# Performance work log

Hardware: AMD Instinct MI355X
Metric: run time of the kernel (lower is better)

## Reference

```python
import jax, jax.numpy as jnp
import numpy as np
from functools import partial

D_MODEL = 1024
D_STATE = 16
D_CONV = 4
EXPAND = 2
DIM = EXPAND * D_MODEL  # 2048


def setup_inputs() -> dict:
    key = jax.random.key(0)
    ks = jax.random.split(key, 10)
    s = lambda fan_in: 1.0 / np.sqrt(fan_in)
    inp = {
        "x": jax.random.normal(ks[0], (8, 2048, D_MODEL), dtype=jnp.float32),
        "W_in": jax.random.normal(ks[1], (DIM, D_MODEL), dtype=jnp.float32) * s(D_MODEL),
        "b_in": jnp.zeros((DIM,), dtype=jnp.float32),
        "conv_w": jax.random.normal(ks[2], (DIM, 1, D_CONV), dtype=jnp.float32) * s(D_CONV),
        "conv_b": jnp.zeros((DIM,), dtype=jnp.float32),
        "W_x": jax.random.normal(ks[3], (3 * D_STATE, DIM), dtype=jnp.float32) * s(DIM),
        "W_dt": jax.random.normal(ks[4], (DIM, D_STATE), dtype=jnp.float32) * s(D_STATE),
        "b_dt": jnp.zeros((DIM,), dtype=jnp.float32),
        "W_out": jax.random.normal(ks[5], (D_MODEL, DIM), dtype=jnp.float32) * s(DIM),
        "b_out": jnp.zeros((D_MODEL,), dtype=jnp.float32),
    }
    return inp


def _selective_scan(xc, delta, A, Bm, Cm):
    # xc, delta: (B, L, DIM); Bm, Cm: (B, L, N); A: (N,)
    Bsz = xc.shape[0]
    h0 = jnp.zeros((Bsz, DIM, D_STATE), dtype=xc.dtype)

    def step(h, inputs):
        xc_t, d_t, b_t, c_t = inputs  # (B,DIM),(B,DIM),(B,N),(B,N)
        h = h * jnp.exp(d_t[:, :, None] * A) + xc_t[:, :, None] * b_t[:, None, :]
        y_t = jnp.einsum("bdn,bn->bd", h, c_t)
        return h, y_t

    tm = lambda a: jnp.swapaxes(a, 0, 1)  # time-major
    _, ys = jax.lax.scan(step, h0, (tm(xc), tm(delta), tm(Bm), tm(Cm)))
    return jnp.swapaxes(ys, 0, 1)  # (B, L, DIM)


def reference(x, W_in, b_in, conv_w, conv_b, W_x, W_dt, b_dt, W_out, b_out):
    A = -jnp.exp(jnp.linspace(0.0, -5.0, D_STATE).astype(x.dtype))  # (N,)
    xp = x @ W_in.T + b_in  # (B, L, DIM)
    # depthwise conv1d, padding=D_CONV-1 on BOTH sides (as torch Conv1d) -> length L+D_CONV-1
    xc = jax.lax.conv_general_dilated(
        jnp.swapaxes(xp, 1, 2), conv_w,
        window_strides=(1,), padding=[(D_CONV - 1, D_CONV - 1)],
        feature_group_count=DIM,
        dimension_numbers=("NCH", "OIH", "NCH"),
    ) + conv_b[None, :, None]
    xc = jnp.swapaxes(xc, 1, 2)  # (B, Lc, DIM)
    x_dbl = xc @ W_x.T  # (B, Lc, 3N)
    d_raw, Bm, Cm = jnp.split(x_dbl, [D_STATE, 2 * D_STATE], axis=-1)
    delta = jax.nn.softplus(d_raw @ W_dt.T + b_dt)  # (B, Lc, DIM)
    y = _selective_scan(xc, delta, A, Bm, Cm)  # (B, Lc, DIM)
    return y @ W_out.T + b_out  # (B, Lc, D_MODEL)
```

## Files before the change

### kernel.cpp

```cpp
#include <hip/hip_runtime.h>
#include <cstdint>
#include <cstddef>

#define B8 8
#define LSEQ 2048
#define LC 2051
#define DMODEL 1024
#define DIM 2048
#define LPAD 2054
#define M2 16408
#define M2P 16512
#define CS 32
#define NCH 65

typedef __attribute__((ext_vector_type(8))) short short8;
typedef __attribute__((ext_vector_type(4))) float floatx4;
typedef __attribute__((ext_vector_type(2))) float float2v;

__device__ __constant__ float AeT[16] = {
  -1.0f,          -0.71653131f, -0.51341712f, -0.36787944f,
  -0.26359714f,   -0.18887560f, -0.13533528f, -0.09697208f,
  -0.06948345f,   -0.04978707f, -0.03567399f, -0.02556154f,
  -0.01831564f,   -0.01312373f, -0.00940356f, -0.00673795f};

#define LOG2E 1.44269504088896f

__device__ __forceinline__ float bf2f(unsigned short h) {
  union { unsigned int u; float f; } v; v.u = ((unsigned int)h) << 16; return v.f;
}
__device__ __forceinline__ unsigned short f2bf(float f) {
  union { float f; unsigned int u; } v; v.f = f;
  unsigned int r = (v.u + 0x7FFFu + ((v.u >> 16) & 1u)) >> 16;
  return (unsigned short)r;
}

__device__ __forceinline__ float2v pk_mul_vv(float2v a, float2v b) {
  float2v d; asm("v_pk_mul_f32 %0, %1, %2" : "=v"(d) : "v"(a), "v"(b)); return d;
}
__device__ __forceinline__ float2v pk_mul_sv(float2v bs, float2v a) {
  float2v d; asm("v_pk_mul_f32 %0, %1, %2" : "=v"(d) : "s"(bs), "v"(a)); return d;
}
__device__ __forceinline__ float2v pk_fma_vvv(float2v a, float2v b, float2v c) {
  float2v d; asm("v_pk_fma_f32 %0, %1, %2, %3" : "=v"(d) : "v"(a), "v"(b), "v"(c)); return d;
}
__device__ __forceinline__ float2v pk_fma_vsv(float2v a, float2v bs, float2v c) {
  float2v d; asm("v_pk_fma_f32 %0, %1, %2, %3" : "=v"(d) : "v"(a), "s"(bs), "v"(c)); return d;
}
__device__ __forceinline__ float2v pk_add_vv(float2v a, float2v b) {
  float2v d; asm("v_pk_add_f32 %0, %1, %2" : "=v"(d) : "v"(a), "v"(b)); return d;
}
__device__ __forceinline__ float exp2_raw(float x) {
  float d; asm("v_exp_f32 %0, %1" : "=v"(d) : "v"(x)); return d;
}

__global__ __launch_bounds__(256) void cvt_f32_bf16(const float* __restrict__ in,
                                                    unsigned short* __restrict__ out,
                                                    int n8) {
  int i = blockIdx.x * 256 + threadIdx.x;
  if (i >= n8) return;
  const float4* p = (const float4*)in + (size_t)i * 2;
  float4 a = p[0], b = p[1];
  uint4 o;
  o.x = (unsigned)f2bf(a.x) | ((unsigned)f2bf(a.y) << 16);
  o.y = (unsigned)f2bf(a.z) | ((unsigned)f2bf(a.w) << 16);
  o.z = (unsigned)f2bf(b.x) | ((unsigned)f2bf(b.y) << 16);
  o.w = (unsigned)f2bf(b.z) | ((unsigned)f2bf(b.w) << 16);
  *((uint4*)out + i) = o;
}

__global__ __launch_bounds__(256) void zero_pads(unsigned short* __restrict__ xp) {
  int i = blockIdx.x * 256 + threadIdx.x;
  int b = i / 1536;
  int r6 = (i % 1536) / 256;
  int dd = (i % 256) * 8;
  int row = (r6 < 3) ? r6 : (2048 + r6);
  uint4 z = make_uint4(0, 0, 0, 0);
  *(uint4*)(xp + ((size_t)b * LPAD + row) * DIM + dd) = z;
}

__global__ __launch_bounds__(256) void conv_kernel(const unsigned short* __restrict__ xp,
                                                   const float* __restrict__ conv_w,
                                                   const float* __restrict__ conv_b,
                                                   unsigned short* __restrict__ xc) {
  const int tc = blockIdx.x, b = blockIdx.y;
  const int d0 = threadIdx.x * 8;
  const unsigned short* base = xp + ((size_t)b * LPAD + tc) * DIM + d0;

  float4 cw[8];
#pragma unroll
  for (int j = 0; j < 8; ++j) cw[j] = *(const float4*)(conv_w + (size_t)(d0 + j) * 4);

  float acc[8];
  const float4* cb4 = (const float4*)(conv_b + d0);
  float4 cb0 = cb4[0], cb1 = cb4[1];
  acc[0] = cb0.x; acc[1] = cb0.y; acc[2] = cb0.z; acc[3] = cb0.w;
  acc[4] = cb1.x; acc[5] = cb1.y; acc[6] = cb1.z; acc[7] = cb1.w;

#pragma unroll
  for (int k = 0; k < 4; ++k) {
    uint4 v = *(const uint4*)(base + (size_t)k * DIM);
    unsigned short e[8];
    e[0] = v.x & 0xffff; e[1] = v.x >> 16; e[2] = v.y & 0xffff; e[3] = v.y >> 16;
    e[4] = v.z & 0xffff; e[5] = v.z >> 16; e[6] = v.w & 0xffff; e[7] = v.w >> 16;
#pragma unroll
    for (int j = 0; j < 8; ++j)
      acc[j] = fmaf(bf2f(e[j]), ((const float*)&cw[j])[k], acc[j]);
  }
  uint4 o;
  o.x = (unsigned)f2bf(acc[0]) | ((unsigned)f2bf(acc[1]) << 16);
  o.y = (unsigned)f2bf(acc[2]) | ((unsigned)f2bf(acc[3]) << 16);
  o.z = (unsigned)f2bf(acc[4]) | ((unsigned)f2bf(acc[5]) << 16);
  o.w = (unsigned)f2bf(acc[6]) | ((unsigned)f2bf(acc[7]) << 16);
  *(uint4*)(xc + ((size_t)b * LC + tc) * DIM + d0) = o;
}

#define GAS(p) ((const __attribute__((address_space(1))) void*)(p))
#define LAS(p) ((__attribute__((address_space(3))) void*)(p))

template <int MODE, int NBM, int NBN, int LX>
__global__ __launch_bounds__(256) void gemm_bt(const unsigned short* __restrict__ A,
                                               const unsigned short* __restrict__ Bw,
                                               const float* __restrict__ bias,
                                               void* __restrict__ Cout, int K) {
  const int gid = blockIdx.x;
  const int xcd = gid & 7;
  const int j = gid >> 3;
  const int bmL = j % LX;
  const int bn = j / LX;
  const int bm = xcd * LX + bmL;
  if (bm >= NBM) return;

  __shared__ __align__(16) short As[128 * 32];
  __shared__ __align__(16) short Bs[128 * 32];
  const int tid = threadIdx.x;
  const int lane = tid & 63, wave = tid >> 6;
  const int wr = wave >> 1, wc = wave & 1;

  floatx4 acc[4][4];
#pragma unroll
  for (int i = 0; i < 4; ++i)
#pragma unroll
    for (int j2 = 0; j2 < 4; ++j2) acc[i][j2] = (floatx4){0.f, 0.f, 0.f, 0.f};

  const int sr = tid >> 2;
  const int sc = (tid & 3) * 8;
  const unsigned short* Ab = A + (size_t)(bm * 128 + sr) * K + sc;
  const unsigned short* Bb = Bw + (size_t)(bn * 128 + sr) * K + sc;
  const size_t rowK64 = (size_t)64 * K;

  const int fr = lane & 15;
  const int fk = (lane >> 4) * 8;
  const int aoff0 = (wr * 64 + fr) * 32 + fk;
  const int boff0 = (wc * 64 + fr) * 32 + fk;

  for (int k0 = 0; k0 < K; k0 += 32) {
    __syncthreads();
    __builtin_amdgcn_global_load_lds(GAS(Ab + k0),          LAS(As + tid * 8), 16, 0, 0);
    __builtin_amdgcn_global_load_lds(GAS(Ab + rowK64 + k0), LAS(As + 2048 + tid * 8), 16, 0, 0);
    __builtin_amdgcn_global_load_lds(GAS(Bb + k0),          LAS(Bs + tid * 8), 16, 0, 0);
    __builtin_amdgcn_global_load_lds(GAS(Bb + rowK64 + k0), LAS(Bs + 2048 + tid * 8), 16, 0, 0);
    __syncthreads();

    short8 af[4], bf[4];
#pragma unroll
    for (int mt = 0; mt < 4; ++mt) af[mt] = *(const short8*)&As[aoff0 + mt * 16 * 32];
#pragma unroll
    for (int nt = 0; nt < 4; ++nt) bf[nt] = *(const short8*)&Bs[boff0 + nt * 16 * 32];
#pragma unroll
    for (int mt = 0; mt < 4; ++mt)
#pragma unroll
      for (int nt = 0; nt < 4; ++nt)
        acc[mt][nt] = __builtin_amdgcn_mfma_f32_16x16x32_bf16(af[mt], bf[nt], acc[mt][nt], 0, 0, 0);
  }

  const int er = (lane >> 4) * 4, ec = lane & 15;
#pragma unroll
  for (int mt = 0; mt < 4; ++mt) {
#pragma unroll
    for (int nt = 0; nt < 4; ++nt) {
#pragma unroll
      for (int i = 0; i < 4; ++i) {
        int r = bm * 128 + wr * 64 + mt * 16 + er + i;
        int c = bn * 128 + wc * 64 + nt * 16 + ec;
        float v = acc[mt][nt][i];
        if constexpr (MODE == 0) {
          int bb = r >> 11, t = r & 2047;
          ((unsigned short*)Cout)[((size_t)bb * LPAD + 3 + t) * DIM + c] = f2bf(v + bias[c]);
        } else if constexpr (MODE == 1) {
          if (r < M2 && c < 48) ((float*)Cout)[(size_t)r * 48 + c] = v;
        } else {
          if (r < M2) ((float*)Cout)[(size_t)r * DMODEL + c] = v + bias[c];
        }
      }
    }
  }
}

__global__ __launch_bounds__(256) void delta_kernel(const float* __restrict__ xdbl,
                                                    const float* __restrict__ W_dt,
                                                    const float* __restrict__ b_dt,
                                                    unsigned short* __restrict__ delta) {
  const int d = blockIdx.y * 256 + threadIdx.x;
  const int r0 = blockIdx.x * 8;
  float wv[16];
  const float4* wp = (const float4*)(W_dt + (size_t)d * 16);
#pragma unroll
  for (int q = 0; q < 4; ++q) {
    float4 t = wp[q];
    wv[q * 4 + 0] = t.x; wv[q * 4 + 1] = t.y; wv[q * 4 + 2] = t.z; wv[q * 4 + 3] = t.w;
  }
  const float bd = b_dt[d];
#pragma unroll
  for (int j = 0; j < 8; ++j) {
    const float* dr = xdbl + (size_t)(r0 + j) * 48;
    float z0 = bd, z1 = 0.f, z2 = 0.f, z3 = 0.f;
#pragma unroll
    for (int n = 0; n < 16; n += 4) {
      z0 = fmaf(dr[n + 0], wv[n + 0], z0);
      z1 = fmaf(dr[n + 1], wv[n + 1], z1);
      z2 = fmaf(dr[n + 2], wv[n + 2], z2);
      z3 = fmaf(dr[n + 3], wv[n + 3], z3);
    }
    float z = (z0 + z1) + (z2 + z3);
    float dl = (z > 20.f) ? z : __logf(1.f + __expf(z));
    delta[(size_t)(r0 + j) * DIM + d] = f2bf(dl);
  }
}

__global__ __launch_bounds__(256) void scan_pass1(const unsigned short* __restrict__ xc,
                                                  const unsigned short* __restrict__ dl,
                                                  const float* __restrict__ xd,
                                                  unsigned short* __restrict__ sdbuf,
                                                  unsigned short* __restrict__ qbuf) {
  const int wid = __builtin_amdgcn_readfirstlane((int)(threadIdx.x >> 6));
  const int lane = threadIdx.x & 63;
  const int W = blockIdx.x * 4 + wid;
  const int dg = W & 31;
  const int rest = W >> 5;
  const int c = rest % NCH;
  const int b = rest / NCH;
  const int d = dg * 64 + lane;
  const int t0 = c * CS;
  const int nst = (t0 + CS <= LC) ? CS : (LC - t0);

  float2v A2L[8];
#pragma unroll
  for (int i = 0; i < 8; ++i)
    A2L[i] = (float2v){AeT[2 * i] * LOG2E, AeT[2 * i + 1] * LOG2E};

  float2v h2[8];
#pragma unroll
  for (int i = 0; i < 8; ++i) h2[i] = (float2v){0.f, 0.f};
  float sumd = 0.f;

  const size_t row0 = (size_t)b * LC + t0;
  const float* xdb = xd + row0 * 48 + 16;
  const unsigned short* xcp = xc + row0 * DIM + d;
  const unsigned short* dp  = dl + row0 * DIM + d;

  float2v BA[8], BB[8];
#pragma unroll
  for (int j = 0; j < 8; ++j) BA[j] = *(const float2v*)(xdb + 2 * j);
  float d0v = bf2f(dp[0]), x0v = bf2f(xcp[0]);

  auto step = [&](const float2v (&Bv)[8], float dlt, float xcv) {
    sumd += dlt;
    float2v dlt2 = (float2v){dlt, dlt};
    float2v xcv2 = (float2v){xcv, xcv};
#pragma unroll
    for (int i = 0; i < 8; ++i) {
      float2v arg = pk_mul_vv(dlt2, A2L[i]);
      float e0 = exp2_raw(arg.x), e1 = exp2_raw(arg.y);
      float2v e2 = (float2v){e0, e1};
      h2[i] = pk_fma_vvv(h2[i], e2, pk_mul_sv(Bv[i], xcv2));
    }
  };

  for (int s = 0; s < nst; s += 2) {
    int s1 = (s + 1 < nst) ? s + 1 : s;
#pragma unroll
    for (int j = 0; j < 8; ++j) BB[j] = *(const float2v*)(xdb + (size_t)s1 * 48 + 2 * j);
    float d1v = bf2f(dp[(size_t)s1 * DIM]);
    float x1v = bf2f(xcp[(size_t)s1 * DIM]);
    step(BA, d0v, x0v);
    if (s + 1 >= nst) break;
    int s2 = (s + 2 < nst) ? s + 2 : s + 1;
#pragma unroll
    for (int j = 0; j < 8; ++j) BA[j] = *(const float2v*)(xdb + (size_t)s2 * 48 + 2 * j);
    d0v = bf2f(dp[(size_t)s2 * DIM]);
    x0v = bf2f(xcp[(size_t)s2 * DIM]);
    step(BB, d1v, x1v);
  }

  sdbuf[((size_t)(b * NCH + c) << 11) + d] = f2bf(sumd);
  const size_t base = ((size_t)(b * NCH + c) * 16) * 2048 + d;
#pragma unroll
  for (int i = 0; i < 8; ++i) {
    qbuf[base + ((size_t)(2 * i) << 11)]     = f2bf(h2[i].x);
    qbuf[base + ((size_t)(2 * i + 1) << 11)] = f2bf(h2[i].y);
  }
}

__global__ __launch_bounds__(64) void scan_boundary(const unsigned short* __restrict__ sdbuf,
                                                    unsigned short* __restrict__ qbuf) {
  const int d = blockIdx.x * 64 + threadIdx.x;
  const int b = blockIdx.y;
  float h[16];
#pragma unroll
  for (int n = 0; n < 16; ++n) h[n] = 0.f;
  for (int c = 0; c < NCH; ++c) {
    const float sd = bf2f(sdbuf[((size_t)(b * NCH + c) << 11) + d]);
    const size_t base = ((size_t)(b * NCH + c) * 16) * 2048 + d;
    float qv[16];
#pragma unroll
    for (int n = 0; n < 16; ++n) qv[n] = bf2f(qbuf[base + ((size_t)n << 11)]);
#pragma unroll
    for (int n = 0; n < 16; ++n) {
      float Pv = __expf(sd * AeT[n]);
      qbuf[base + ((size_t)n << 11)] = f2bf(h[n]);
      h[n] = fmaf(Pv, h[n], qv[n]);
    }
  }
}

__global__ __launch_bounds__(256) void scan_pass2(const unsigned short* __restrict__ xc,
                                                  const unsigned short* __restrict__ dl,
                                                  const float* __restrict__ xd,
                                                  const unsigned short* __restrict__ hinit,
                                                  unsigned short* __restrict__ y) {
  const int wid = __builtin_amdgcn_readfirstlane((int)(threadIdx.x >> 6));
  const int lane = threadIdx.x & 63;
  const int W = blockIdx.x * 4 + wid;
  const int dg = W & 31;
  const int rest = W >> 5;
  const int c = rest % NCH;
  const int b = rest / NCH;
  const int d = dg * 64 + lane;
  const int t0 = c * CS;
  const int nst = (t0 + CS <= LC) ? CS : (LC - t0);

  float2v A2L[8];
#pragma unroll
  for (int i = 0; i < 8; ++i)
    A2L[i] = (float2v){AeT[2 * i] * LOG2E, AeT[2 * i + 1] * LOG2E};

  const size_t base = ((size_t)(b * NCH + c) * 16) * 2048 + d;
  float2v h2[8];
#pragma unroll
  for (int i = 0; i < 8; ++i)
    h2[i] = (float2v){bf2f(hinit[base + ((size_t)(2 * i) << 11)]),
                      bf2f(hinit[base + ((size_t)(2 * i + 1) << 11)])};

  const size_t row0 = (size_t)b * LC + t0;
  const float* xdb = xd + row0 * 48 + 16;
  const unsigned short* xcp = xc + row0 * DIM + d;
  const unsigned short* dp  = dl + row0 * DIM + d;
  unsigned short* yp = y + row0 * DIM + d;

  float2v BA[8], CA[8], BB[8], CB[8];
#pragma unroll
  for (int j = 0; j < 8; ++j) {
    BA[j] = *(const float2v*)(xdb + 2 * j);
    CA[j] = *(const float2v*)(xdb + 16 + 2 * j);
  }
  float d0v = bf2f(dp[0]), x0v = bf2f(xcp[0]);

  auto step = [&](const float2v (&Bv)[8], const float2v (&Cv)[8], float dlt, float xcv, int s) {
    float2v dlt2 = (float2v){dlt, dlt};
    float2v xcv2 = (float2v){xcv, xcv};
    float2v y2[4];
#pragma unroll
    for (int i = 0; i < 4; ++i) y2[i] = (float2v){0.f, 0.f};
#pragma unroll
    for (int i = 0; i < 8; ++i) {
      float2v arg = pk_mul_vv(dlt2, A2L[i]);
      float e0 = exp2_raw(arg.x), e1 = exp2_raw(arg.y);
      float2v e2 = (float2v){e0, e1};
      h2[i] = pk_fma_vvv(h2[i], e2, pk_mul_sv(Bv[i], xcv2));
      y2[i & 3] = pk_fma_vsv(h2[i], Cv[i], y2[i & 3]);
    }
    float2v s01 = pk_add_vv(y2[0], y2[1]);
    float2v s23 = pk_add_vv(y2[2], y2[3]);
    float2v st = pk_add_vv(s01, s23);
    yp[(size_t)s * DIM] = f2bf(st.x + st.y);
  };

  for (int s = 0; s < nst; s += 2) {
    int s1 = (s + 1 < nst) ? s + 1 : s;
#pragma unroll
    for (int j = 0; j < 8; ++j) {
      BB[j] = *(const float2v*)(xdb + (size_t)s1 * 48 + 2 * j);
      CB[j] = *(const float2v*)(xdb + (size_t)s1 * 48 + 16 + 2 * j);
    }
    float d1v = bf2f(dp[(size_t)s1 * DIM]);
    float x1v = bf2f(xcp[(size_t)s1 * DIM]);
    step(BA, CA, d0v, x0v, s);
    if (s + 1 >= nst) break;
    int s2 = (s + 2 < nst) ? s + 2 : s + 1;
#pragma unroll
    for (int j = 0; j < 8; ++j) {
      BA[j] = *(const float2v*)(xdb + (size_t)s2 * 48 + 2 * j);
      CA[j] = *(const float2v*)(xdb + (size_t)s2 * 48 + 16 + 2 * j);
    }
    d0v = bf2f(dp[(size_t)s2 * DIM]);
    x0v = bf2f(xcp[(size_t)s2 * DIM]);
    step(BB, CB, d1v, x1v, s + 1);
  }
}

extern "C" void kernel_launch(void* const* d_in, const int* in_sizes, int n_in,
                              void* d_out, int out_size, void* d_ws, size_t ws_size,
                              hipStream_t stream) {
  const float* x      = (const float*)d_in[0];
  const float* W_in   = (const float*)d_in[1];
  const float* b_in   = (const float*)d_in[2];
  const float* conv_w = (const float*)d_in[3];
  const float* conv_b = (const float*)d_in[4];
  const float* W_x    = (const float*)d_in[5];
  const float* W_dt   = (const float*)d_in[6];
  const float* b_dt   = (const float*)d_in[7];
  const float* W_out  = (const float*)d_in[8];
  const float* b_out  = (const float*)d_in[9];

  char* w = (char*)d_ws;
  unsigned short* xp    = (unsigned short*)w;
  unsigned short* delta = (unsigned short*)w;
  unsigned short* ybuf  = (unsigned short*)w;
  size_t off = (size_t)M2P * DIM * 2;
  unsigned short* xcb  = (unsigned short*)(w + off); off += (size_t)M2P * DIM * 2;
  size_t xA_off = off;
  unsigned short* xA   = (unsigned short*)(w + off); off += (size_t)16384 * 1024 * 2;
  unsigned short* wInB = (unsigned short*)(w + off); off += (size_t)2048 * 1024 * 2;
  unsigned short* wOutB= (unsigned short*)(w + off); off += (size_t)1024 * 2048 * 2;
  unsigned short* wXB  = (unsigned short*)(w + off); off += (size_t)128 * 2048 * 2;
  float* xdbl          = (float*)(w + off);          off += (size_t)M2 * 48 * 4;
  unsigned short* sdbuf = (unsigned short*)(w + xA_off);
  unsigned short* qbuf  = (unsigned short*)(w + xA_off + (size_t)B8 * NCH * 2048 * 2);
  (void)ws_size; (void)in_sizes; (void)n_in; (void)out_size;

  cvt_f32_bf16<<<8192, 256, 0, stream>>>(x, xA, 2097152);
  cvt_f32_bf16<<<1024, 256, 0, stream>>>(W_in, wInB, 262144);
  cvt_f32_bf16<<<1024, 256, 0, stream>>>(W_out, wOutB, 262144);
  cvt_f32_bf16<<<48,   256, 0, stream>>>(W_x, wXB, 12288);
  zero_pads<<<48, 256, 0, stream>>>(xp);

  gemm_bt<0, 128, 16, 16><<<2048, 256, 0, stream>>>(xA, wInB, b_in, xp, 1024);
  conv_kernel<<<dim3(LC, B8), 256, 0, stream>>>(xp, conv_w, conv_b, xcb);
  gemm_bt<1, 129, 1, 17><<<136, 256, 0, stream>>>(xcb, wXB, nullptr, xdbl, 2048);
  delta_kernel<<<dim3(2051, 8), 256, 0, stream>>>(xdbl, W_dt, b_dt, delta);

  scan_pass1<<<4160, 256, 0, stream>>>(xcb, delta, xdbl, sdbuf, qbuf);
  scan_boundary<<<dim3(32, B8), 64, 0, stream>>>(sdbuf, qbuf);
  scan_pass2<<<4160, 256, 0, stream>>>(xcb, delta, xdbl, qbuf, ybuf);

  gemm_bt<2, 129, 8, 17><<<1088, 256, 0, stream>>>(ybuf, wOutB, b_out, (float*)d_out, 2048);
}
```

Baseline: 614.3 us.

## Add 256x256 tile GEMM with 4-stage direct-to-LDS pipeline for in/out projections

Introduces a new GEMM kernel with 512 threads, 256x256 output tiles, swizzled LDS layout and a 4-deep ring of global_load_lds stages with split barriers and MFMA priority hints. It replaces the input and output projection GEMMs, while the old gemm_bt is kept only for the small x_dbl projection. The larger tiles raise data reuse and the deeper prefetch overlaps memory with MFMA, in exchange for higher register and LDS pressure and fewer blocks, which may leave CUs idle on the out-projection grid.

```diff
diff --git a/kernel.cpp b/kernel.cpp
--- a/kernel.cpp
+++ b/kernel.cpp
@@ -117,10 +117,9 @@
 #define GAS(p) ((const __attribute__((address_space(1))) void*)(p))
 #define LAS(p) ((__attribute__((address_space(3))) void*)(p))
 
-template <int MODE, int NBM, int NBN, int LX>
+template <int NBM, int NBN, int LX>
 __global__ __launch_bounds__(256) void gemm_bt(const unsigned short* __restrict__ A,
                                                const unsigned short* __restrict__ Bw,
-                                               const float* __restrict__ bias,
                                                void* __restrict__ Cout, int K) {
   const int gid = blockIdx.x;
   const int xcd = gid & 7;
@@ -183,11 +182,143 @@
         int r = bm * 128 + wr * 64 + mt * 16 + er + i;
         int c = bn * 128 + wc * 64 + nt * 16 + ec;
         float v = acc[mt][nt][i];
+        if (r < M2 && c < 48) ((float*)Cout)[(size_t)r * 48 + c] = v;
+      }
+    }
+  }
+}
+
+template <int MODE, int NBM, int NBN, int LX, int NT>
+__global__ __launch_bounds__(512, 2) void gemm8p(const unsigned short* __restrict__ A,
+                                                 const unsigned short* __restrict__ Bw,
+                                                 const float* __restrict__ bias,
+                                                 void* __restrict__ Cout) {
+  constexpr int K = NT * 32;
+  const int gid = blockIdx.x;
+  const int xcd = gid & 7;
+  const int jj = gid >> 3;
+  const int bm = xcd * LX + (jj % LX);
+  const int bn = jj / LX;
+  if (bm >= NBM) return;
+
+  __shared__ __align__(16) unsigned short lds[4][2][8192];
+
+  const int tid = threadIdx.x;
+  const int lane = tid & 63;
+  const int wid = tid >> 6;
+  const int wr = wid >> 2;
+  const int wc = wid & 3;
+
+  const int srow0 = tid >> 2;
+  const int logb0 = (tid & 3) ^ (srow0 & 3);
+  const unsigned short* Asrc0 = A  + (size_t)(bm * 256 + srow0)       * K + logb0 * 8;
+  const unsigned short* Asrc1 = A  + (size_t)(bm * 256 + 128 + srow0) * K + logb0 * 8;
+  const unsigned short* Bsrc0 = Bw + (size_t)(bn * 256 + srow0)       * K + logb0 * 8;
+  const unsigned short* Bsrc1 = Bw + (size_t)(bn * 256 + 128 + srow0) * K + logb0 * 8;
+
+  const int fr = lane & 15;
+  const int xorb = ((lane >> 4) ^ (lane & 3)) * 8;
+  int offA[8], offB[4];
+#pragma unroll
+  for (int m = 0; m < 8; ++m) offA[m] = (wr * 128 + m * 16 + fr) * 32 + xorb;
+#pragma unroll
+  for (int n = 0; n < 4; ++n) offB[n] = (wc * 64 + n * 16 + fr) * 32 + xorb;
+
+  floatx4 acc[8][4];
+#pragma unroll
+  for (int m = 0; m < 8; ++m)
+#pragma unroll
+    for (int n = 0; n < 4; ++n) acc[m][n] = (floatx4){0.f, 0.f, 0.f, 0.f};
+
+  auto STAGE = [&](int tile, int mat) {
+    unsigned short* db = &lds[tile & 3][mat][0];
+    const unsigned short* s0 = mat ? Bsrc0 : Asrc0;
+    const unsigned short* s1 = mat ? Bsrc1 : Asrc1;
+    __builtin_amdgcn_global_load_lds(GAS(s0 + (size_t)tile * 32), LAS(db + tid * 8), 16, 0, 0);
+    __builtin_amdgcn_global_load_lds(GAS(s1 + (size_t)tile * 32), LAS(db + 4096 + tid * 8), 16, 0, 0);
+  };
+
+#pragma unroll
+  for (int t = 0; t < 3; ++t) {
+    if (t < NT) { STAGE(t, 0); STAGE(t, 1); }
+  }
+
+  for (int t = 0; t < NT; ++t) {
+    const unsigned short* ldsA = &lds[t & 3][0][0];
+    const unsigned short* ldsB = &lds[t & 3][1][0];
+    asm volatile("s_waitcnt vmcnt(8)" ::: "memory");
+    __builtin_amdgcn_s_barrier();
+    if (t + 3 < NT) STAGE(t + 3, 0);
+    short8 b0 = *(const short8*)&ldsB[offB[0]];
+    short8 b1 = *(const short8*)&ldsB[offB[1]];
+    short8 b2 = *(const short8*)&ldsB[offB[2]];
+    short8 b3 = *(const short8*)&ldsB[offB[3]];
+    {
+      short8 a0 = *(const short8*)&ldsA[offA[0]];
+      short8 a1 = *(const short8*)&ldsA[offA[1]];
+      short8 a2 = *(const short8*)&ldsA[offA[2]];
+      short8 a3 = *(const short8*)&ldsA[offA[3]];
+      __builtin_amdgcn_s_setprio(1);
+      acc[0][0] = __builtin_amdgcn_mfma_f32_16x16x32_bf16(a0, b0, acc[0][0], 0, 0, 0);
+      acc[0][1] = __builtin_amdgcn_mfma_f32_16x16x32_bf16(a0, b1, acc[0][1], 0, 0, 0);
+      acc[0][2] = __builtin_amdgcn_mfma_f32_16x16x32_bf16(a0, b2, acc[0][2], 0, 0, 0);
+      acc[0][3] = __builtin_amdgcn_mfma_f32_16x16x32_bf16(a0, b3, acc[0][3], 0, 0, 0);
+      acc[1][0] = __builtin_amdgcn_mfma_f32_16x16x32_bf16(a1, b0, acc[1][0], 0, 0, 0);
+      acc[1][1] = __builtin_amdgcn_mfma_f32_16x16x32_bf16(a1, b1, acc[1][1], 0, 0, 0);
+      acc[1][2] = __builtin_amdgcn_mfma_f32_16x16x32_bf16(a1, b2, acc[1][2], 0, 0, 0);
+      acc[1][3] = __builtin_amdgcn_mfma_f32_16x16x32_bf16(a1, b3, acc[1][3], 0, 0, 0);
+      acc[2][0] = __builtin_amdgcn_mfma_f32_16x16x32_bf16(a2, b0, acc[2][0], 0, 0, 0);
+      acc[2][1] = __builtin_amdgcn_mfma_f32_16x16x32_bf16(a2, b1, acc[2][1], 0, 0, 0);
+      acc[2][2] = __builtin_amdgcn_mfma_f32_16x16x32_bf16(a2, b2, acc[2][2], 0, 0, 0);
+      acc[2][3] = __builtin_amdgcn_mfma_f32_16x16x32_bf16(a2, b3, acc[2][3], 0, 0, 0);
+      acc[3][0] = __builtin_amdgcn_mfma_f32_16x16x32_bf16(a3, b0, acc[3][0], 0, 0, 0);
+      acc[3][1] = __builtin_amdgcn_mfma_f32_16x16x32_bf16(a3, b1, acc[3][1], 0, 0, 0);
+      acc[3][2] = __builtin_amdgcn_mfma_f32_16x16x32_bf16(a3, b2, acc[3][2], 0, 0, 0);
+      acc[3][3] = __builtin_amdgcn_mfma_f32_16x16x32_bf16(a3, b3, acc[3][3], 0, 0, 0);
+      __builtin_amdgcn_s_setprio(0);
+    }
+    asm volatile("s_waitcnt vmcnt(8)" ::: "memory");
+    __builtin_amdgcn_s_barrier();
+    if (t + 3 < NT) STAGE(t + 3, 1);
+    {
+      short8 a4 = *(const short8*)&ldsA[offA[4]];
+      short8 a5 = *(const short8*)&ldsA[offA[5]];
+      short8 a6 = *(const short8*)&ldsA[offA[6]];
+      short8 a7 = *(const short8*)&ldsA[offA[7]];
+      __builtin_amdgcn_s_setprio(1);
+      acc[4][0] = __builtin_amdgcn_mfma_f32_16x16x32_bf16(a4, b0, acc[4][0], 0, 0, 0);
+      acc[4][1] = __builtin_amdgcn_mfma_f32_16x16x32_bf16(a4, b1, acc[4][1], 0, 0, 0);
+      acc[4][2] = __builtin_amdgcn_mfma_f32_16x16x32_bf16(a4, b2, acc[4][2], 0, 0, 0);
+      acc[4][3] = __builtin_amdgcn_mfma_f32_16x16x32_bf16(a4, b3, acc[4][3], 0, 0, 0);
+      acc[5][0] = __builtin_amdgcn_mfma_f32_16x16x32_bf16(a5, b0, acc[5][0], 0, 0, 0);
+      acc[5][1] = __builtin_amdgcn_mfma_f32_16x16x32_bf16(a5, b1, acc[5][1], 0, 0, 0);
+      acc[5][2] = __builtin_amdgcn_mfma_f32_16x16x32_bf16(a5, b2, acc[5][2], 0, 0, 0);
+      acc[5][3] = __builtin_amdgcn_mfma_f32_16x16x32_bf16(a5, b3, acc[5][3], 0, 0, 0);
+      acc[6][0] = __builtin_amdgcn_mfma_f32_16x16x32_bf16(a6, b0, acc[6][0], 0, 0, 0);
+      acc[6][1] = __builtin_amdgcn_mfma_f32_16x16x32_bf16(a6, b1, acc[6][1], 0, 0, 0);
+      acc[6][2] = __builtin_amdgcn_mfma_f32_16x16x32_bf16(a6, b2, acc[6][2], 0, 0, 0);
+      acc[6][3] = __builtin_amdgcn_mfma_f32_16x16x32_bf16(a6, b3, acc[6][3], 0, 0, 0);
+      acc[7][0] = __builtin_amdgcn_mfma_f32_16x16x32_bf16(a7, b0, acc[7][0], 0, 0, 0);
+      acc[7][1] = __builtin_amdgcn_mfma_f32_16x16x32_bf16(a7, b1, acc[7][1], 0, 0, 0);
+      acc[7][2] = __builtin_amdgcn_mfma_f32_16x16x32_bf16(a7, b2, acc[7][2], 0, 0, 0);
+      acc[7][3] = __builtin_amdgcn_mfma_f32_16x16x32_bf16(a7, b3, acc[7][3], 0, 0, 0);
+      __builtin_amdgcn_s_setprio(0);
+    }
+  }
+
+  const int er = (lane >> 4) * 4, ec = lane & 15;
+#pragma unroll
+  for (int m = 0; m < 8; ++m) {
+#pragma unroll
+    for (int n = 0; n < 4; ++n) {
+#pragma unroll
+      for (int i = 0; i < 4; ++i) {
+        int r = bm * 256 + wr * 128 + m * 16 + er + i;
+        int c = bn * 256 + wc * 64 + n * 16 + ec;
+        float v = acc[m][n][i];
         if constexpr (MODE == 0) {
-          int bb = r >> 11, t = r & 2047;
-          ((unsigned short*)Cout)[((size_t)bb * LPAD + 3 + t) * DIM + c] = f2bf(v + bias[c]);
-        } else if constexpr (MODE == 1) {
-          if (r < M2 && c < 48) ((float*)Cout)[(size_t)r * 48 + c] = v;
+          int bb = r >> 11, tt = r & 2047;
+          ((unsigned short*)Cout)[((size_t)bb * LPAD + 3 + tt) * DIM + c] = f2bf(v + bias[c]);
         } else {
           if (r < M2) ((float*)Cout)[(size_t)r * DMODEL + c] = v + bias[c];
         }
@@ -444,14 +575,14 @@
   cvt_f32_bf16<<<48,   256, 0, stream>>>(W_x, wXB, 12288);
   zero_pads<<<48, 256, 0, stream>>>(xp);
 
-  gemm_bt<0, 128, 16, 16><<<2048, 256, 0, stream>>>(xA, wInB, b_in, xp, 1024);
+  gemm8p<0, 64, 8, 8, 32><<<512, 512, 0, stream>>>(xA, wInB, b_in, xp);
   conv_kernel<<<dim3(LC, B8), 256, 0, stream>>>(xp, conv_w, conv_b, xcb);
-  gemm_bt<1, 129, 1, 17><<<136, 256, 0, stream>>>(xcb, wXB, nullptr, xdbl, 2048);
+  gemm_bt<129, 1, 17><<<136, 256, 0, stream>>>(xcb, wXB, xdbl, 2048);
   delta_kernel<<<dim3(2051, 8), 256, 0, stream>>>(xdbl, W_dt, b_dt, delta);
 
   scan_pass1<<<4160, 256, 0, stream>>>(xcb, delta, xdbl, sdbuf, qbuf);
   scan_boundary<<<dim3(32, B8), 64, 0, stream>>>(sdbuf, qbuf);
   scan_pass2<<<4160, 256, 0, stream>>>(xcb, delta, xdbl, qbuf, ybuf);
 
-  gemm_bt<2, 129, 8, 17><<<1088, 256, 0, stream>>>(ybuf, wOutB, b_out, (float*)d_out, 2048);
-}
+  gemm8p<2, 65, 4, 9, 64><<<288, 512, 0, stream>>>(ybuf, wOutB, b_out, (float*)d_out);
+}
```

After: 617.4 us. About the same (+0.5%).

## Add 256x256-tile 8-wave GEMM with 4-stage LDS pipeline for in/out projections

Applied to the files above, without the earlier changes.

Introduces a new GEMM kernel with 256x256 output tiles, 512 threads (8 waves each holding 128x64 accumulators), a 4-deep global_load_lds prefetch ring with swizzled LDS layout, and explicit waitcnt/setprio scheduling. The input and output projections now use it, while the small x_dbl GEMM keeps the old kernel. The larger tiles raise reuse of A and B per LDS load and overlap loads with MFMA. The cost is high register pressure and only 288 blocks for the output GEMM, which with 65 row tiles and padding may leave the GPU underfilled.

```diff
diff --git a/kernel.cpp b/kernel.cpp
--- a/kernel.cpp
+++ b/kernel.cpp
@@ -16,6 +16,7 @@
 typedef __attribute__((ext_vector_type(8))) short short8;
 typedef __attribute__((ext_vector_type(4))) float floatx4;
 typedef __attribute__((ext_vector_type(2))) float float2v;
+typedef __attribute__((address_space(3))) unsigned short lds_ushort;
 
 __device__ __constant__ float AeT[16] = {
   -1.0f,          -0.71653131f, -0.51341712f, -0.36787944f,
@@ -51,6 +52,13 @@
 }
 __device__ __forceinline__ float exp2_raw(float x) {
   float d; asm("v_exp_f32 %0, %1" : "=v"(d) : "v"(x)); return d;
+}
+
+__device__ __forceinline__ short8 ds_read_b128_(const lds_ushort* p) {
+  floatx4 d;
+  unsigned addr = (unsigned)(size_t)p;
+  asm volatile("ds_read_b128 %0, %1" : "=v"(d) : "v"(addr));
+  return __builtin_bit_cast(short8, d);
 }
 
 __global__ __launch_bounds__(256) void cvt_f32_bf16(const float* __restrict__ in,
@@ -117,10 +125,9 @@
 #define GAS(p) ((const __attribute__((address_space(1))) void*)(p))
 #define LAS(p) ((__attribute__((address_space(3))) void*)(p))
 
-template <int MODE, int NBM, int NBN, int LX>
+template <int NBM, int NBN, int LX>
 __global__ __launch_bounds__(256) void gemm_bt(const unsigned short* __restrict__ A,
                                                const unsigned short* __restrict__ Bw,
-                                               const float* __restrict__ bias,
                                                void* __restrict__ Cout, int K) {
   const int gid = blockIdx.x;
   const int xcd = gid & 7;
@@ -183,11 +190,105 @@
         int r = bm * 128 + wr * 64 + mt * 16 + er + i;
         int c = bn * 128 + wc * 64 + nt * 16 + ec;
         float v = acc[mt][nt][i];
+        if (r < M2 && c < 48) ((float*)Cout)[(size_t)r * 48 + c] = v;
+      }
+    }
+  }
+}
+
+template <int MODE, int NBM, int NBN, int LX, int NT>
+__global__ __launch_bounds__(512, 2) void gemm8p(const unsigned short* __restrict__ A,
+                                                 const unsigned short* __restrict__ Bw,
+                                                 const float* __restrict__ bias,
+                                                 void* __restrict__ Cout) {
+  constexpr int K = NT * 32;
+  const int gid = blockIdx.x;
+  const int xcd = gid & 7;
+  const int jj = gid >> 3;
+  const int bm = xcd * LX + (jj % LX);
+  const int bn = jj / LX;
+  if (bm >= NBM) return;
+
+  __shared__ __align__(16) unsigned short lds[4][2][8192];
+
+  const int tid = threadIdx.x;
+  const int lane = tid & 63;
+  const int wid = tid >> 6;
+  const int wr = wid >> 2;
+  const int wc = wid & 3;
+
+  const int srow = tid >> 2;
+  const int sblk = (tid & 3) ^ ((tid >> 3) & 3);
+  const unsigned short* As0 = A  + (size_t)(bm * 256 + srow)       * K + sblk * 8;
+  const unsigned short* As1 = A  + (size_t)(bm * 256 + 128 + srow) * K + sblk * 8;
+  const unsigned short* Bs0 = Bw + (size_t)(bn * 256 + srow)       * K + sblk * 8;
+  const unsigned short* Bs1 = Bw + (size_t)(bn * 256 + 128 + srow) * K + sblk * 8;
+
+  const int fr = lane & 15;
+  const int physb = (lane >> 4) ^ ((lane >> 1) & 3);
+  int offA[8], offB[4];
+#pragma unroll
+  for (int m = 0; m < 8; ++m) offA[m] = (wr * 128 + m * 16 + fr) * 32 + physb * 8;
+#pragma unroll
+  for (int n = 0; n < 4; ++n) offB[n] = (wc * 64 + n * 16 + fr) * 32 + physb * 8;
+
+  floatx4 acc[8][4];
+#pragma unroll
+  for (int m = 0; m < 8; ++m)
+#pragma unroll
+    for (int n = 0; n < 4; ++n) acc[m][n] = (floatx4){0.f, 0.f, 0.f, 0.f};
+
+  auto STAGE = [&](int t) {
+    const int koff = t * 32;
+    unsigned short* dA = &lds[t & 3][0][0];
+    unsigned short* dB = &lds[t & 3][1][0];
+    __builtin_amdgcn_global_load_lds(GAS(As0 + koff), LAS(dA + tid * 8), 16, 0, 0);
+    __builtin_amdgcn_global_load_lds(GAS(As1 + koff), LAS(dA + 4096 + tid * 8), 16, 0, 0);
+    __builtin_amdgcn_global_load_lds(GAS(Bs0 + koff), LAS(dB + tid * 8), 16, 0, 0);
+    __builtin_amdgcn_global_load_lds(GAS(Bs1 + koff), LAS(dB + 4096 + tid * 8), 16, 0, 0);
+  };
+
+  STAGE(0); STAGE(1); STAGE(2);
+
+  for (int t = 0; t < NT; ++t) {
+    if (t + 2 < NT)      asm volatile("s_waitcnt vmcnt(8)");
+    else if (t + 1 < NT) asm volatile("s_waitcnt vmcnt(4)");
+    else                 asm volatile("s_waitcnt vmcnt(0)");
+    __builtin_amdgcn_s_barrier();
+    if (t + 3 < NT) STAGE(t + 3);
+
+    const lds_ushort* tA = (const lds_ushort*)LAS(&lds[t & 3][0][0]);
+    const lds_ushort* tB = (const lds_ushort*)LAS(&lds[t & 3][1][0]);
+    short8 bf[4], af[8];
+#pragma unroll
+    for (int n = 0; n < 4; ++n) bf[n] = ds_read_b128_(tB + offB[n]);
+#pragma unroll
+    for (int m = 0; m < 8; ++m) af[m] = ds_read_b128_(tA + offA[m]);
+    asm volatile("s_waitcnt lgkmcnt(0)");
+    __builtin_amdgcn_sched_barrier(0);
+
+    __builtin_amdgcn_s_setprio(1);
+#pragma unroll
+    for (int m = 0; m < 8; ++m)
+#pragma unroll
+      for (int n = 0; n < 4; ++n)
+        acc[m][n] = __builtin_amdgcn_mfma_f32_16x16x32_bf16(af[m], bf[n], acc[m][n], 0, 0, 0);
+    __builtin_amdgcn_s_setprio(0);
+  }
+
+  const int er = (lane >> 4) * 4, ec = lane & 15;
+#pragma unroll
+  for (int m = 0; m < 8; ++m) {
+#pragma unroll
+    for (int n = 0; n < 4; ++n) {
+#pragma unroll
+      for (int i = 0; i < 4; ++i) {
+        int r = bm * 256 + wr * 128 + m * 16 + er + i;
+        int c = bn * 256 + wc * 64 + n * 16 + ec;
+        float v = acc[m][n][i];
         if constexpr (MODE == 0) {
-          int bb = r >> 11, t = r & 2047;
-          ((unsigned short*)Cout)[((size_t)bb * LPAD + 3 + t) * DIM + c] = f2bf(v + bias[c]);
-        } else if constexpr (MODE == 1) {
-          if (r < M2 && c < 48) ((float*)Cout)[(size_t)r * 48 + c] = v;
+          int bb = r >> 11, tt = r & 2047;
+          ((unsigned short*)Cout)[((size_t)bb * LPAD + 3 + tt) * DIM + c] = f2bf(v + bias[c]);
         } else {
           if (r < M2) ((float*)Cout)[(size_t)r * DMODEL + c] = v + bias[c];
         }
@@ -444,14 +545,14 @@
   cvt_f32_bf16<<<48,   256, 0, stream>>>(W_x, wXB, 12288);
   zero_pads<<<48, 256, 0, stream>>>(xp);
 
-  gemm_bt<0, 128, 16, 16><<<2048, 256, 0, stream>>>(xA, wInB, b_in, xp, 1024);
+  gemm8p<0, 64, 8, 8, 32><<<512, 512, 0, stream>>>(xA, wInB, b_in, xp);
   conv_kernel<<<dim3(LC, B8), 256, 0, stream>>>(xp, conv_w, conv_b, xcb);
-  gemm_bt<1, 129, 1, 17><<<136, 256, 0, stream>>>(xcb, wXB, nullptr, xdbl, 2048);
+  gemm_bt<129, 1, 17><<<136, 256, 0, stream>>>(xcb, wXB, xdbl, 2048);
   delta_kernel<<<dim3(2051, 8), 256, 0, stream>>>(xdbl, W_dt, b_dt, delta);
 
   scan_pass1<<<4160, 256, 0, stream>>>(xcb, delta, xdbl, sdbuf, qbuf);
   scan_boundary<<<dim3(32, B8), 64, 0, stream>>>(sdbuf, qbuf);
   scan_pass2<<<4160, 256, 0, stream>>>(xcb, delta, xdbl, qbuf, ybuf);
 
-  gemm_bt<2, 129, 8, 17><<<1088, 256, 0, stream>>>(ybuf, wOutB, b_out, (float*)d_out, 2048);
-}
+  gemm8p<2, 65, 4, 9, 64><<<288, 512, 0, stream>>>(ybuf, wOutB, b_out, (float*)d_out);
+}
```

Result: no change. 612.3 us (-0.3%).

## Double GEMM K-tile to 64 with XOR-swizzled LDS and parallelize scan boundary

Applied to the files above, without the earlier changes.

The GEMM now stages a 128x64 K slice per iteration, using an XOR swizzle on the LDS column to avoid bank conflicts, and runs two MFMA sub-steps per barrier pair. This halves the number of syncthreads and load rounds per K. Separately, scan_boundary spreads the 16 state lanes across threads: 256-thread blocks with one state per thread instead of 64 threads each holding 16 states. This gives far more parallelism for the sequential chunk-carry pass. LDS use doubles to 32KB per block, which may reduce occupancy.

```diff
diff --git a/kernel.cpp b/kernel.cpp
--- a/kernel.cpp
+++ b/kernel.cpp
@@ -125,13 +125,12 @@
   const int gid = blockIdx.x;
   const int xcd = gid & 7;
   const int j = gid >> 3;
-  const int bmL = j % LX;
+  const int bm = xcd * LX + (j % LX);
   const int bn = j / LX;
-  const int bm = xcd * LX + bmL;
   if (bm >= NBM) return;
 
-  __shared__ __align__(16) short As[128 * 32];
-  __shared__ __align__(16) short Bs[128 * 32];
+  __shared__ __align__(16) unsigned short As[128 * 64];
+  __shared__ __align__(16) unsigned short Bs[128 * 64];
   const int tid = threadIdx.x;
   const int lane = tid & 63, wave = tid >> 6;
   const int wr = wave >> 1, wc = wave & 1;
@@ -142,35 +141,43 @@
 #pragma unroll
     for (int j2 = 0; j2 < 4; ++j2) acc[i][j2] = (floatx4){0.f, 0.f, 0.f, 0.f};
 
-  const int sr = tid >> 2;
-  const int sc = (tid & 3) * 8;
-  const unsigned short* Ab = A + (size_t)(bm * 128 + sr) * K + sc;
-  const unsigned short* Bb = Bw + (size_t)(bn * 128 + sr) * K + sc;
-  const size_t rowK64 = (size_t)64 * K;
+  const int srow = tid >> 3;
+  const int scol = ((tid & 7) ^ ((tid >> 3) & 7)) * 8;
+  const unsigned short* Ab[4];
+  const unsigned short* Bb[4];
+#pragma unroll
+  for (int L = 0; L < 4; ++L) {
+    Ab[L] = A  + (size_t)(bm * 128 + L * 32 + srow) * K + scol;
+    Bb[L] = Bw + (size_t)(bn * 128 + L * 32 + srow) * K + scol;
+  }
 
   const int fr = lane & 15;
-  const int fk = (lane >> 4) * 8;
-  const int aoff0 = (wr * 64 + fr) * 32 + fk;
-  const int boff0 = (wc * 64 + fr) * 32 + fk;
-
-  for (int k0 = 0; k0 < K; k0 += 32) {
+  const int hi = lane >> 4;
+  const int fx = fr & 7;
+
+  for (int k0 = 0; k0 < K; k0 += 64) {
     __syncthreads();
-    __builtin_amdgcn_global_load_lds(GAS(Ab + k0),          LAS(As + tid * 8), 16, 0, 0);
-    __builtin_amdgcn_global_load_lds(GAS(Ab + rowK64 + k0), LAS(As + 2048 + tid * 8), 16, 0, 0);
-    __builtin_amdgcn_global_load_lds(GAS(Bb + k0),          LAS(Bs + tid * 8), 16, 0, 0);
-    __builtin_amdgcn_global_load_lds(GAS(Bb + rowK64 + k0), LAS(Bs + 2048 + tid * 8), 16, 0, 0);
+#pragma unroll
+    for (int L = 0; L < 4; ++L) {
+      __builtin_amdgcn_global_load_lds(GAS(Ab[L] + k0), LAS(As + L * 2048 + tid * 8), 16, 0, 0);
+      __builtin_amdgcn_global_load_lds(GAS(Bb[L] + k0), LAS(Bs + L * 2048 + tid * 8), 16, 0, 0);
+    }
     __syncthreads();
 
-    short8 af[4], bf[4];
-#pragma unroll
-    for (int mt = 0; mt < 4; ++mt) af[mt] = *(const short8*)&As[aoff0 + mt * 16 * 32];
-#pragma unroll
-    for (int nt = 0; nt < 4; ++nt) bf[nt] = *(const short8*)&Bs[boff0 + nt * 16 * 32];
-#pragma unroll
-    for (int mt = 0; mt < 4; ++mt)
-#pragma unroll
-      for (int nt = 0; nt < 4; ++nt)
-        acc[mt][nt] = __builtin_amdgcn_mfma_f32_16x16x32_bf16(af[mt], bf[nt], acc[mt][nt], 0, 0, 0);
+#pragma unroll
+    for (int kk = 0; kk < 2; ++kk) {
+      const int pb = ((kk * 4 + hi) ^ fx) * 8;
+      short8 af[4], bf[4];
+#pragma unroll
+      for (int mt = 0; mt < 4; ++mt) af[mt] = *(const short8*)&As[(wr * 64 + mt * 16 + fr) * 64 + pb];
+#pragma unroll
+      for (int nt = 0; nt < 4; ++nt) bf[nt] = *(const short8*)&Bs[(wc * 64 + nt * 16 + fr) * 64 + pb];
+#pragma unroll
+      for (int mt = 0; mt < 4; ++mt)
+#pragma unroll
+        for (int nt = 0; nt < 4; ++nt)
+          acc[mt][nt] = __builtin_amdgcn_mfma_f32_16x16x32_bf16(af[mt], bf[nt], acc[mt][nt], 0, 0, 0);
+    }
   }
 
   const int er = (lane >> 4) * 4, ec = lane & 15;
@@ -301,25 +308,22 @@
   }
 }
 
-__global__ __launch_bounds__(64) void scan_boundary(const unsigned short* __restrict__ sdbuf,
-                                                    unsigned short* __restrict__ qbuf) {
-  const int d = blockIdx.x * 64 + threadIdx.x;
+__global__ __launch_bounds__(256) void scan_boundary(const unsigned short* __restrict__ sdbuf,
+                                                     unsigned short* __restrict__ qbuf) {
+  const int tid = threadIdx.x;
+  const int n = tid >> 4;
+  const int d = blockIdx.x * 16 + (tid & 15);
   const int b = blockIdx.y;
-  float h[16];
-#pragma unroll
-  for (int n = 0; n < 16; ++n) h[n] = 0.f;
+  const float aL = AeT[n] * LOG2E;
+  float h = 0.f;
   for (int c = 0; c < NCH; ++c) {
-    const float sd = bf2f(sdbuf[((size_t)(b * NCH + c) << 11) + d]);
-    const size_t base = ((size_t)(b * NCH + c) * 16) * 2048 + d;
-    float qv[16];
-#pragma unroll
-    for (int n = 0; n < 16; ++n) qv[n] = bf2f(qbuf[base + ((size_t)n << 11)]);
-#pragma unroll
-    for (int n = 0; n < 16; ++n) {
-      float Pv = __expf(sd * AeT[n]);
-      qbuf[base + ((size_t)n << 11)] = f2bf(h[n]);
-      h[n] = fmaf(Pv, h[n], qv[n]);
-    }
+    const size_t sbase = ((size_t)(b * NCH + c) << 11);
+    const float sd = bf2f(sdbuf[sbase + d]);
+    const size_t base = (sbase << 4) + ((size_t)n << 11) + d;
+    const float qv = bf2f(qbuf[base]);
+    const float Pv = exp2_raw(sd * aL);
+    qbuf[base] = f2bf(h);
+    h = fmaf(Pv, h, qv);
   }
 }
 
@@ -450,7 +454,7 @@
   delta_kernel<<<dim3(2051, 8), 256, 0, stream>>>(xdbl, W_dt, b_dt, delta);
 
   scan_pass1<<<4160, 256, 0, stream>>>(xcb, delta, xdbl, sdbuf, qbuf);
-  scan_boundary<<<dim3(32, B8), 64, 0, stream>>>(sdbuf, qbuf);
+  scan_boundary<<<dim3(128, B8), 256, 0, stream>>>(sdbuf, qbuf);
   scan_pass2<<<4160, 256, 0, stream>>>(xcb, delta, xdbl, qbuf, ybuf);
 
   gemm_bt<2, 129, 8, 17><<<1088, 256, 0, stream>>>(ybuf, wOutB, b_out, (float*)d_out, 2048);
```

Result: faster. 579.6 us (-5.6%).
